# Kernel tuning notes

Hardware: AMD Instinct MI355X
Metric: run time of the kernel (lower is better)

Reference implementation:

```python
import jax, jax.numpy as jnp
import numpy as np

B, D, K = 64, 8732, 81
RATIO = 1.0

def setup_inputs() -> dict:
    key = jax.random.key(0)
    k1, k2, k3, k4 = jax.random.split(key, 4)
    return {
        'loc_preds': jax.random.normal(k1, (B, D, 4), dtype=jnp.float32),
        'loc_targets': jax.random.normal(k2, (B, D, 4), dtype=jnp.float32),
        'conf_preds': jax.random.normal(k3, (B, D, K), dtype=jnp.float32),
        'conf_targets': jax.random.randint(k4, (B, D), 0, K, dtype=jnp.int32),
    }

def reference(loc_preds, loc_targets, conf_preds, conf_targets):
    b, d, k = conf_preds.shape
    pos = conf_targets > 0                                  # [B, D] bool
    num_matched = jnp.sum(pos).astype(conf_preds.dtype)     # scalar (python float in torch)
    num_matched = jax.lax.stop_gradient(num_matched)

    # --- localization smooth-L1 over positive boxes only ---
    z = jnp.abs(loc_preds - loc_targets)
    sl1 = jnp.where(z < 1.0, 0.5 * z * z, z - 0.5)          # [B, D, 4]
    loc_loss = jnp.sum(sl1 * pos[..., None].astype(sl1.dtype))

    # --- per-box CE (custom: GLOBAL max for stability), detached, for mining ---
    x = conf_preds.reshape(-1, k)                           # [B*D, K]
    y = conf_targets.reshape(-1)                            # [B*D]
    xmax = jnp.max(x)                                       # x.data.max() in torch (global scalar)
    lse = jnp.log(jnp.sum(jnp.exp(x - xmax), axis=1)) + xmax
    ce_mine = lse - jnp.take_along_axis(x, y[:, None].astype(jnp.int32), axis=1)[:, 0]
    conf_loss_mat = jax.lax.stop_gradient(ce_mine).reshape(b, d)

    # --- hard negative mining: double argsort rank trick ---
    cl = jnp.where(pos, 0.0, conf_loss_mat)                 # conf_loss[pos] = 0
    idx = jnp.argsort(-cl, axis=1)                          # descending sort indices
    rank = jnp.argsort(idx, axis=1)                         # rank of each box
    num_pos = jnp.sum(pos, axis=1, keepdims=True).astype(jnp.float32)   # [B,1]
    num_neg = jnp.minimum(3.0 * RATIO * num_pos, float(d - 1))          # clamp max=D-1
    neg = rank.astype(jnp.float32) < num_neg                # [B, D] bool

    # --- final confidence loss: standard CE summed over pos | neg ---
    sel = (pos | neg).reshape(-1)                           # [B*D]
    logp = jax.nn.log_softmax(x, axis=1)
    ce = -jnp.take_along_axis(logp, y[:, None].astype(jnp.int32), axis=1)[:, 0]
    conf_loss = jnp.sum(jnp.where(sel, ce, 0.0))

    loc_loss = loc_loss / num_matched
    conf_loss = conf_loss / num_matched
    return (loc_loss + conf_loss, conf_loss, loc_loss)
```

## Files before the change

### kernel.cpp

```cpp
#include <hip/hip_runtime.h>
#include <math.h>

constexpr int BB = 64;
constexpr int DD = 8732;
constexpr int KK = 81;
constexpr int NBOX = BB * DD;
constexpr int SL = 137;
constexpr int NPART = BB * SL;

__device__ inline float smooth_l1(float d) {
    float z = fabsf(d);
    return z < 1.0f ? 0.5f * z * z : z - 0.5f;
}

__global__ void __launch_bounds__(256) fused_kernel(
    const float4* __restrict__ lp, const float4* __restrict__ lt,
    const float* __restrict__ cp, const int* __restrict__ ct,
    float* __restrict__ ce, int* __restrict__ cnt_part,
    float* __restrict__ ce_part, float* __restrict__ loc_part)
{
    int tid = threadIdx.x;
    int slice = blockIdx.x, row = blockIdx.y;
    int bir = slice * 64 + (tid >> 2);
    int q = tid & 3;
    bool active = bir < DD;
    float ce_c = 0.0f, locs = 0.0f;
    int c = 0;
    if (active) {
        size_t g = (size_t)row * DD + bir;
        const float* rowp = cp + g * KK;
        const float4* r4 = (const float4*)rowp;
        float4 f[5];
        #pragma unroll
        for (int t = 0; t < 5; ++t) f[t] = r4[q + 4 * t];
        float v80 = rowp[80];

        float m = -INFINITY;
        #pragma unroll
        for (int t = 0; t < 5; ++t)
            m = fmaxf(m, fmaxf(fmaxf(f[t].x, f[t].y), fmaxf(f[t].z, f[t].w)));
        if (q == 0) m = fmaxf(m, v80);
        m = fmaxf(m, __shfl_xor(m, 1));
        m = fmaxf(m, __shfl_xor(m, 2));

        float s = 0.0f;
        #pragma unroll
        for (int t = 0; t < 5; ++t)
            s += __expf(f[t].x - m) + __expf(f[t].y - m)
               + __expf(f[t].z - m) + __expf(f[t].w - m);
        if (q == 0) s += __expf(v80 - m);
        s += __shfl_xor(s, 1);
        s += __shfl_xor(s, 2);

        int y = ct[g];
        float xv = rowp[y];
        float cev = __logf(s) + m - xv;
        if (q == 0) { ce[g] = cev; ce_c = cev; }
        if (q == 1 && y > 0) {
            c = 1;
            float4 a = lp[g], b = lt[g];
            locs = smooth_l1(a.x - b.x) + smooth_l1(a.y - b.y)
                 + smooth_l1(a.z - b.z) + smooth_l1(a.w - b.w);
        }
    }
    for (int o = 32; o; o >>= 1) {
        locs += __shfl_down(locs, o);
        ce_c += __shfl_down(ce_c, o);
        c    += __shfl_down(c, o);
    }
    __shared__ float s_l[4], s_e[4];
    __shared__ int   s_c[4];
    int lane = tid & 63, wid = tid >> 6;
    if (lane == 0) { s_l[wid] = locs; s_e[wid] = ce_c; s_c[wid] = c; }
    __syncthreads();
    if (tid == 0) {
        int idx = row * SL + slice;
        loc_part[idx] = s_l[0] + s_l[1] + s_l[2] + s_l[3];
        ce_part[idx]  = s_e[0] + s_e[1] + s_e[2] + s_e[3];
        cnt_part[idx] = s_c[0] + s_c[1] + s_c[2] + s_c[3];
    }
}

__global__ void __launch_bounds__(256) mine_kernel(
    const int* __restrict__ cnt_part, const float* __restrict__ ce_part,
    const float* __restrict__ ce, const int* __restrict__ ct,
    double* __restrict__ row_conf)
{
    __shared__ double s_d[4];
    __shared__ int s_i[4];
    __shared__ int s_np;
    __shared__ double s_tot;
    __shared__ float cl[DD];
    int r = blockIdx.x, tid = threadIdx.x;
    int lane = tid & 63, wid = tid >> 6;

    int cnt = 0; double tot = 0.0;
    if (tid < SL) { cnt = cnt_part[r * SL + tid]; tot = (double)ce_part[r * SL + tid]; }
    for (int o = 32; o; o >>= 1) { cnt += __shfl_down(cnt, o); tot += __shfl_down(tot, o); }
    if (lane == 0) { s_i[wid] = cnt; s_d[wid] = tot; }
    __syncthreads();
    if (tid == 0) {
        s_np  = s_i[0] + s_i[1] + s_i[2] + s_i[3];
        s_tot = s_d[0] + s_d[1] + s_d[2] + s_d[3];
    }
    __syncthreads();
    int num_pos = s_np;
    float numneg = fminf(3.0f * (float)num_pos, (float)(DD - 1));
    int M = DD - num_pos;
    if ((float)M <= numneg) {
        if (tid == 0) row_conf[r] = s_tot;
        return;
    }
    const int* ctr = ct + r * DD;
    const float* cer = ce + r * DD;
    double sum = 0.0;
    for (int j = tid; j < DD; j += 256) cl[j] = (ctr[j] > 0) ? 0.0f : cer[j];
    __syncthreads();
    for (int i = tid; i < DD; i += 256) {
        if (ctr[i] > 0) { sum += (double)cer[i]; continue; }
        float ci = cl[i];
        int rk = 0;
        for (int j = 0; j < DD; j++) {
            float cj = cl[j];
            rk += (cj > ci || (cj == ci && j < i)) ? 1 : 0;
        }
        if ((float)rk < numneg) sum += (double)cer[i];
    }
    for (int o = 32; o; o >>= 1) sum += __shfl_down(sum, o);
    if (lane == 0) s_d[wid] = sum;
    __syncthreads();
    if (tid == 0) row_conf[r] = s_d[0] + s_d[1] + s_d[2] + s_d[3];
}

__global__ void __launch_bounds__(256) fin_kernel(
    const float* __restrict__ loc_part, const int* __restrict__ cnt_part,
    const double* __restrict__ row_conf, float* __restrict__ out)
{
    int tid = threadIdx.x;
    double l = 0.0, n = 0.0, cf = 0.0;
    for (int j = tid; j < NPART; j += 256) {
        l += (double)loc_part[j];
        n += (double)cnt_part[j];
    }
    if (tid < BB) cf = row_conf[tid];
    for (int o = 32; o; o >>= 1) {
        l  += __shfl_down(l, o);
        cf += __shfl_down(cf, o);
        n  += __shfl_down(n, o);
    }
    __shared__ double sl[4], sc[4], sn[4];
    int lane = tid & 63, wid = tid >> 6;
    if (lane == 0) { sl[wid] = l; sc[wid] = cf; sn[wid] = n; }
    __syncthreads();
    if (tid == 0) {
        double L = sl[0] + sl[1] + sl[2] + sl[3];
        double C = sc[0] + sc[1] + sc[2] + sc[3];
        double N = sn[0] + sn[1] + sn[2] + sn[3];
        out[0] = (float)(L / N + C / N);
        out[1] = (float)(C / N);
        out[2] = (float)(L / N);
    }
}

extern "C" void kernel_launch(void* const* d_in, const int* in_sizes, int n_in,
                              void* d_out, int out_size, void* d_ws, size_t ws_size,
                              hipStream_t stream) {
    const float4* lp = (const float4*)d_in[0];
    const float4* lt = (const float4*)d_in[1];
    const float* cp = (const float*)d_in[2];
    const int* ct = (const int*)d_in[3];
    float* out = (float*)d_out;

    char* w = (char*)d_ws;
    int*    cnt_part = (int*)w;
    float*  loc_part = (float*)(w + 35072);
    float*  ce_part  = (float*)(w + 70144);
    double* row_conf = (double*)(w + 105216);
    float*  ce       = (float*)(w + 105728);

    dim3 grid(SL, BB);
    fused_kernel<<<grid, 256, 0, stream>>>(lp, lt, cp, ct, ce,
                                           cnt_part, ce_part, loc_part);
    mine_kernel<<<BB, 256, 0, stream>>>(cnt_part, ce_part, ce, ct, row_conf);
    fin_kernel<<<1, 256, 0, stream>>>(loc_part, cnt_part, row_conf, out);
}
```

Baseline: 48.38 us.

## Merge mining and final reduction into one single-block kernel; nontemporal stores

Replaces the per-row mine kernel and the final reduction kernel with one 1024-thread single-block kernel. It reduces per-row positive counts and CE sums, and runs the O(D^2) rank-based mining only for rows whose negative budget does not cover all negatives, processing those rows one after another. It also switches the CE store and the loc loads to nontemporal variants. This saves a kernel launch, but any row that needs full mining now runs serially on one workgroup rather than in parallel across 64 blocks.

```diff
diff --git a/kernel.cpp b/kernel.cpp
--- a/kernel.cpp
+++ b/kernel.cpp
@@ -8,13 +8,15 @@
 constexpr int SL = 137;
 constexpr int NPART = BB * SL;
 
+typedef float f4 __attribute__((ext_vector_type(4)));
+
 __device__ inline float smooth_l1(float d) {
     float z = fabsf(d);
     return z < 1.0f ? 0.5f * z * z : z - 0.5f;
 }
 
 __global__ void __launch_bounds__(256) fused_kernel(
-    const float4* __restrict__ lp, const float4* __restrict__ lt,
+    const f4* __restrict__ lp, const f4* __restrict__ lt,
     const float* __restrict__ cp, const int* __restrict__ ct,
     float* __restrict__ ce, int* __restrict__ cnt_part,
     float* __restrict__ ce_part, float* __restrict__ loc_part)
@@ -29,8 +31,8 @@
     if (active) {
         size_t g = (size_t)row * DD + bir;
         const float* rowp = cp + g * KK;
-        const float4* r4 = (const float4*)rowp;
-        float4 f[5];
+        const f4* r4 = (const f4*)rowp;
+        f4 f[5];
         #pragma unroll
         for (int t = 0; t < 5; ++t) f[t] = r4[q + 4 * t];
         float v80 = rowp[80];
@@ -55,10 +57,11 @@
         int y = ct[g];
         float xv = rowp[y];
         float cev = __logf(s) + m - xv;
-        if (q == 0) { ce[g] = cev; ce_c = cev; }
+        if (q == 0) { __builtin_nontemporal_store(cev, ce + g); ce_c = cev; }
         if (q == 1 && y > 0) {
             c = 1;
-            float4 a = lp[g], b = lt[g];
+            f4 a = __builtin_nontemporal_load(lp + g);
+            f4 b = __builtin_nontemporal_load(lt + g);
             locs = smooth_l1(a.x - b.x) + smooth_l1(a.y - b.y)
                  + smooth_l1(a.z - b.z) + smooth_l1(a.w - b.w);
         }
@@ -81,81 +84,86 @@
     }
 }
 
-__global__ void __launch_bounds__(256) mine_kernel(
+__global__ void __launch_bounds__(1024) finish_kernel(
     const int* __restrict__ cnt_part, const float* __restrict__ ce_part,
-    const float* __restrict__ ce, const int* __restrict__ ct,
-    double* __restrict__ row_conf)
+    const float* __restrict__ loc_part, const float* __restrict__ ce,
+    const int* __restrict__ ct, float* __restrict__ out)
 {
-    __shared__ double s_d[4];
-    __shared__ int s_i[4];
-    __shared__ int s_np;
-    __shared__ double s_tot;
+    __shared__ int s_np[BB];
+    __shared__ double s_ce[BB];
+    __shared__ double s_l[16], s_n[16], s_fs[16];
+    __shared__ double s_conf;
+    __shared__ int s_fb[BB], s_nfb;
     __shared__ float cl[DD];
-    int r = blockIdx.x, tid = threadIdx.x;
+
+    int tid = threadIdx.x;
     int lane = tid & 63, wid = tid >> 6;
+    int row = tid >> 4, sub = tid & 15;
 
-    int cnt = 0; double tot = 0.0;
-    if (tid < SL) { cnt = cnt_part[r * SL + tid]; tot = (double)ce_part[r * SL + tid]; }
-    for (int o = 32; o; o >>= 1) { cnt += __shfl_down(cnt, o); tot += __shfl_down(tot, o); }
-    if (lane == 0) { s_i[wid] = cnt; s_d[wid] = tot; }
-    __syncthreads();
-    if (tid == 0) {
-        s_np  = s_i[0] + s_i[1] + s_i[2] + s_i[3];
-        s_tot = s_d[0] + s_d[1] + s_d[2] + s_d[3];
+    int np = 0; double ces = 0.0;
+    for (int s = sub; s < SL; s += 16) {
+        int idx = row * SL + s;
+        np += cnt_part[idx];
+        ces += (double)ce_part[idx];
     }
-    __syncthreads();
-    int num_pos = s_np;
-    float numneg = fminf(3.0f * (float)num_pos, (float)(DD - 1));
-    int M = DD - num_pos;
-    if ((float)M <= numneg) {
-        if (tid == 0) row_conf[r] = s_tot;
-        return;
-    }
-    const int* ctr = ct + r * DD;
-    const float* cer = ce + r * DD;
-    double sum = 0.0;
-    for (int j = tid; j < DD; j += 256) cl[j] = (ctr[j] > 0) ? 0.0f : cer[j];
-    __syncthreads();
-    for (int i = tid; i < DD; i += 256) {
-        if (ctr[i] > 0) { sum += (double)cer[i]; continue; }
-        float ci = cl[i];
-        int rk = 0;
-        for (int j = 0; j < DD; j++) {
-            float cj = cl[j];
-            rk += (cj > ci || (cj == ci && j < i)) ? 1 : 0;
-        }
-        if ((float)rk < numneg) sum += (double)cer[i];
-    }
-    for (int o = 32; o; o >>= 1) sum += __shfl_down(sum, o);
-    if (lane == 0) s_d[wid] = sum;
-    __syncthreads();
-    if (tid == 0) row_conf[r] = s_d[0] + s_d[1] + s_d[2] + s_d[3];
-}
+    for (int o = 8; o; o >>= 1) { np += __shfl_down(np, o); ces += __shfl_down(ces, o); }
+    if (sub == 0) { s_np[row] = np; s_ce[row] = ces; }
 
-__global__ void __launch_bounds__(256) fin_kernel(
-    const float* __restrict__ loc_part, const int* __restrict__ cnt_part,
-    const double* __restrict__ row_conf, float* __restrict__ out)
-{
-    int tid = threadIdx.x;
-    double l = 0.0, n = 0.0, cf = 0.0;
-    for (int j = tid; j < NPART; j += 256) {
+    double l = 0.0, n = 0.0;
+    for (int j = tid; j < NPART; j += 1024) {
         l += (double)loc_part[j];
         n += (double)cnt_part[j];
     }
-    if (tid < BB) cf = row_conf[tid];
-    for (int o = 32; o; o >>= 1) {
-        l  += __shfl_down(l, o);
-        cf += __shfl_down(cf, o);
-        n  += __shfl_down(n, o);
+    for (int o = 32; o; o >>= 1) { l += __shfl_down(l, o); n += __shfl_down(n, o); }
+    if (lane == 0) { s_l[wid] = l; s_n[wid] = n; }
+    __syncthreads();
+
+    if (tid == 0) {
+        double conf = 0.0; int nfb = 0;
+        for (int r = 0; r < BB; ++r) {
+            float numneg = fminf(3.0f * (float)s_np[r], (float)(DD - 1));
+            int M = DD - s_np[r];
+            if ((float)M <= numneg) conf += s_ce[r];
+            else s_fb[nfb++] = r;
+        }
+        s_conf = conf; s_nfb = nfb;
     }
-    __shared__ double sl[4], sc[4], sn[4];
-    int lane = tid & 63, wid = tid >> 6;
-    if (lane == 0) { sl[wid] = l; sc[wid] = cf; sn[wid] = n; }
     __syncthreads();
+
+    for (int fi = 0; fi < s_nfb; ++fi) {
+        int r = s_fb[fi];
+        float numneg = fminf(3.0f * (float)s_np[r], (float)(DD - 1));
+        const int* ctr = ct + r * DD;
+        const float* cer = ce + r * DD;
+        double sum = 0.0;
+        for (int j = tid; j < DD; j += 1024) cl[j] = (ctr[j] > 0) ? 0.0f : cer[j];
+        __syncthreads();
+        for (int i = tid; i < DD; i += 1024) {
+            float cei = cer[i];
+            if (ctr[i] > 0) { sum += (double)cei; continue; }
+            float ci = cl[i];
+            int rk = 0;
+            for (int j = 0; j < DD; j++) {
+                float cj = cl[j];
+                rk += (cj > ci || (cj == ci && j < i)) ? 1 : 0;
+            }
+            if ((float)rk < numneg) sum += (double)cei;
+        }
+        for (int o = 32; o; o >>= 1) sum += __shfl_down(sum, o);
+        if (lane == 0) s_fs[wid] = sum;
+        __syncthreads();
+        if (tid == 0) {
+            double t = 0.0;
+            for (int k = 0; k < 16; ++k) t += s_fs[k];
+            s_conf += t;
+        }
+        __syncthreads();
+    }
+
     if (tid == 0) {
-        double L = sl[0] + sl[1] + sl[2] + sl[3];
-        double C = sc[0] + sc[1] + sc[2] + sc[3];
-        double N = sn[0] + sn[1] + sn[2] + sn[3];
+        double L = 0.0, N = 0.0;
+        for (int k = 0; k < 16; ++k) { L += s_l[k]; N += s_n[k]; }
+        double C = s_conf;
         out[0] = (float)(L / N + C / N);
         out[1] = (float)(C / N);
         out[2] = (float)(L / N);
@@ -165,8 +173,8 @@
 extern "C" void kernel_launch(void* const* d_in, const int* in_sizes, int n_in,
                               void* d_out, int out_size, void* d_ws, size_t ws_size,
                               hipStream_t stream) {
-    const float4* lp = (const float4*)d_in[0];
-    const float4* lt = (const float4*)d_in[1];
+    const f4* lp = (const f4*)d_in[0];
+    const f4* lt = (const f4*)d_in[1];
     const float* cp = (const float*)d_in[2];
     const int* ct = (const int*)d_in[3];
     float* out = (float*)d_out;
@@ -175,12 +183,10 @@
     int*    cnt_part = (int*)w;
     float*  loc_part = (float*)(w + 35072);
     float*  ce_part  = (float*)(w + 70144);
-    double* row_conf = (double*)(w + 105216);
-    float*  ce       = (float*)(w + 105728);
+    float*  ce       = (float*)(w + 105216);
 
     dim3 grid(SL, BB);
     fused_kernel<<<grid, 256, 0, stream>>>(lp, lt, cp, ct, ce,
                                            cnt_part, ce_part, loc_part);
-    mine_kernel<<<BB, 256, 0, stream>>>(cnt_part, ce_part, ce, ct, row_conf);
-    fin_kernel<<<1, 256, 0, stream>>>(loc_part, cnt_part, row_conf, out);
+    finish_kernel<<<1, 1024, 0, stream>>>(cnt_part, ce_part, loc_part, ce, ct, out);
 }
```

New measurement: 50.38 us. 4.1% more time.
